# Performance work log

Hardware: AMD Instinct MI355X
Metric: run time of the kernel (lower is better)

## Reference

```python
import jax, jax.numpy as jnp
import numpy as np

B, T, HOP = 4, 200, 120
N = T * HOP
M1, A1 = 40, 5            # mcep_order+1, apdc_order+1
HID, COND = 256, 192
SR = 24000.0
ALPHA = 0.466             # frequency-warping for 24 kHz
PD = 4                    # Pade order
PADE = jnp.asarray([1.0, 0.4999273, 0.1067005, 0.00956526, 0.0003041358], jnp.float32)
SIGN = jnp.asarray([1.0, -1.0, 1.0, -1.0], jnp.float32)  # + for odd Pade tap index
F0_MEAN, F0_STD = 5.0, 0.25
MCEP_MEAN, MCEP_STD = 0.0, 1.0
APDC_MEAN, APDC_STD = 0.0, 1.0
NOISE_RATIO, SP_RATE, F0_RATE = 0.5, 1.0, 1.0


def mc2b(mc, a):
    """SPTK mc2b: mel-cepstrum -> MLSA filter coefficients (scan over order)."""
    mc_rev = jnp.moveaxis(mc, -1, 0)[::-1]  # [M1, B, T]
    def step(carry, c):
        b = c - a * carry
        return b, b
    _, bs = jax.lax.scan(step, jnp.zeros_like(mc_rev[0]), mc_rev)
    return jnp.moveaxis(bs[::-1], 0, -1)


def _mlsafir(x, b, d):
    # SPTK mlsafir, vectorized over the PD Pade taps.
    # x: [PD], b: [M1], d: [PD, M1+1]
    aa = 1.0 - ALPHA * ALPHA
    d1 = aa * x + ALPHA * d[:, 1]
    def step(prev, di):  # d_new[i] = d[i] + a*(d[i+1] - d_new[i-1]) : order recurrence
        d_i, d_ip1 = di
        new = d_i + ALPHA * (d_ip1 - prev)
        return new, new
    xs = (d[:, 2:M1].T, d[:, 3:M1 + 1].T)  # [M1-2, PD]
    _, dupd = jax.lax.scan(step, d1, xs)    # [M1-2, PD]
    y = jnp.einsum('mp,m->p', dupd, b[2:])
    # delay-line shift: new d = [x, d1, d1, dupd[2..M]]
    new_d = jnp.concatenate([x[:, None], d1[:, None], d1[:, None], dupd.T], axis=1)
    return y, new_d


def _mlsa_step(state, inp):
    d1a, d1b, d2, pt2 = state
    x, b = inp
    x = x * jnp.exp(b[0])           # gain
    # ---- stage 1 (uses b[1] only), SPTK mlsadf1 ----
    aa = 1.0 - ALPHA * ALPHA
    na = aa * d1b[:PD] + ALPHA * d1a[1:]
    npt = na * b[1]
    v1 = npt * PADE[1:]
    x1 = x + jnp.sum(v1 * SIGN)
    y1 = jnp.sum(v1) + x1
    d1a = jnp.concatenate([d1a[:1], na])
    d1b = jnp.concatenate([x1[None], npt])
    # ---- stage 2 (orders >= 2), SPTK mlsadf2 ----
    fy, d2 = _mlsafir(pt2[:PD], b, d2)
    v2 = fy * PADE[1:]
    x2 = y1 + jnp.sum(v2 * SIGN)
    y2 = jnp.sum(v2) + x2
    pt2 = jnp.concatenate([x2[None], fy])
    return (d1a, d1b, d2, pt2), y2


def mlsa_filter(exc, b_up):
    # exc: [N], b_up: [N, M1] -> filtered waveform [N]
    init = (jnp.zeros(PD + 1, jnp.float32), jnp.zeros(PD + 1, jnp.float32),
            jnp.zeros((PD, M1 + 1), jnp.float32), jnp.zeros(PD + 1, jnp.float32))
    _, y = jax.lax.scan(_mlsa_step, init, (exc, b_up))
    return y


def _forward(mceps, apdcs, frame_f0s, noise,
             Wm, bm, Wa, ba, Wf, bf, Wpa, bpa, Wpp, bpp,
             Wrp, brp, Wra, bra, Wap):
    # linear feature embed + sum
    hs = mceps @ Wm + bm + apdcs @ Wa + ba + frame_f0s @ Wf + bf   # [B,T,HID]
    ca = hs @ Wpa + bpa                                             # prenet_a cond [B,T,COND]
    cp = hs @ Wpp + bpp                                             # prenet_p cond
    # denorm (+ exp for log-f0)
    f0 = jnp.exp(frame_f0s[..., 0] * F0_STD + F0_MEAN) * F0_RATE    # [B,T]
    sp = mceps * MCEP_STD + MCEP_MEAN
    ap = apdcs * APDC_STD + APDC_MEAN
    # per-path mel-cepstra with prenet residuals
    mc_p = sp * SP_RATE + 0.1 * jnp.tanh(cp @ Wrp + brp)
    mc_a = sp * SP_RATE + 0.1 * jnp.tanh(ca @ Wra + bra) + ap @ Wap
    b_p = mc2b(mc_p, ALPHA)
    b_a = mc2b(mc_a, ALPHA)
    # excitation at sample rate
    f0_up = jnp.repeat(f0, HOP, axis=1)                             # [B,N]
    phase = jnp.cumsum(f0_up / SR, axis=1)
    w = jnp.floor(phase)
    wprev = jnp.concatenate([jnp.zeros_like(w[:, :1]), w[:, :-1]], axis=1)
    amp = jnp.sqrt(SR / jnp.maximum(f0_up, 1.0))
    pulse = jnp.where(w > wprev, amp, 0.0)
    exc_p = pulse * (1.0 - NOISE_RATIO)
    exc_a = noise * NOISE_RATIO
    # run both (periodic/aperiodic) MLSA synthesis filters in one batched scan
    excs = jnp.concatenate([exc_p, exc_a], axis=0)                  # [2B,N]
    bs = jnp.repeat(jnp.concatenate([b_p, b_a], axis=0), HOP, axis=1)  # [2B,N,M1]
    wavs = jax.vmap(mlsa_filter)(excs, bs)                          # [2B,N]
    return wavs[:B] + wavs[B:]


_forward_jit = jax.jit(_forward)


def setup_inputs() -> dict:
    key = jax.random.key(0)
    ks = jax.random.split(key, 20)
    decay = 0.3 / (1.0 + jnp.arange(M1, dtype=jnp.float32))  # realistic cepstral decay (filter stability)
    return {
        'mceps': jax.random.normal(ks[0], (B, T, M1), jnp.float32) * decay,
        'apdcs': jax.random.normal(ks[1], (B, T, A1), jnp.float32) * 0.3,
        'frame_f0s': jax.random.normal(ks[2], (B, T, 1), jnp.float32),
        'noise': jax.random.normal(ks[3], (B, N), jnp.float32),
        'Wm': jax.random.normal(ks[4], (M1, HID), jnp.float32) / np.sqrt(M1),
        'bm': jnp.zeros((HID,), jnp.float32),
        'Wa': jax.random.normal(ks[5], (A1, HID), jnp.float32) / np.sqrt(A1),
        'ba': jnp.zeros((HID,), jnp.float32),
        'Wf': jax.random.normal(ks[6], (1, HID), jnp.float32),
        'bf': jnp.zeros((HID,), jnp.float32),
        'Wpa': jax.random.normal(ks[7], (HID, COND), jnp.float32) / np.sqrt(HID),
        'bpa': jnp.zeros((COND,), jnp.float32),
        'Wpp': jax.random.normal(ks[8], (HID, COND), jnp.float32) / np.sqrt(HID),
        'bpp': jnp.zeros((COND,), jnp.float32),
        'Wrp': jax.random.normal(ks[9], (COND, M1), jnp.float32) / np.sqrt(COND),
        'brp': jnp.zeros((M1,), jnp.float32),
        'Wra': jax.random.normal(ks[10], (COND, M1), jnp.float32) / np.sqrt(COND),
        'bra': jnp.zeros((M1,), jnp.float32),
        'Wap': jax.random.normal(ks[11], (A1, M1), jnp.float32) * 0.05,
    }


def reference(mceps, apdcs, frame_f0s, noise,
              Wm, bm, Wa, ba, Wf, bf, Wpa, bpa, Wpp, bpp,
              Wrp, brp, Wra, bra, Wap):
    return _forward_jit(mceps, apdcs, frame_f0s, noise,
                        Wm, bm, Wa, ba, Wf, bf, Wpa, bpa, Wpp, bpp,
                        Wrp, brp, Wra, bra, Wap)
```

## Files before the change

kernel.cpp:

```cpp
#include <hip/hip_runtime.h>
#include <math.h>

#define ALPHA 0.466f
#define T_FRAMES 200
#define HOPW 120
#define NSAMP 24000
#define M1 40
#define HID 256
#define CONDW 192

#define WARMS 384
#define OUTS 96
#define SLOTS (NSAMP / OUTS)

#define F8 8
#define EMB_BLOCKS (4 * T_FRAMES / F8)
#define BPF ((NSAMP + 255) / 256)

#if defined(__has_builtin)
#  if __has_builtin(__builtin_amdgcn_permlane32_swap)
#    define HAVE_PLSWAP 1
#  endif
#endif
#ifndef HAVE_PLSWAP
#  define HAVE_PLSWAP 0
#endif

__global__ __launch_bounds__(256) void prep_kernel(
    const float* __restrict__ mceps, const float* __restrict__ apdcs,
    const float* __restrict__ f0s, const float* __restrict__ noise,
    const float* __restrict__ Wm, const float* __restrict__ bm,
    const float* __restrict__ Wa, const float* __restrict__ ba,
    const float* __restrict__ Wf, const float* __restrict__ bf,
    const float* __restrict__ Wpa, const float* __restrict__ bpa,
    const float* __restrict__ Wpp, const float* __restrict__ bpp,
    const float* __restrict__ Wrp, const float* __restrict__ brp,
    const float* __restrict__ Wra, const float* __restrict__ bra,
    const float* __restrict__ Wap,
    float* __restrict__ bcoef, float* __restrict__ exc)
{
    const int tid = threadIdx.x;

    if (blockIdx.x >= EMB_BLOCKS) {
        const int xb = blockIdx.x - EMB_BLOCKS;
        const int ff = xb / BPF;
        const int n = (xb % BPF) * 256 + tid;

        if (ff >= 4) {
            if (n < NSAMP) exc[ff * NSAMP + n] = 0.5f * noise[(ff - 4) * NSAMP + n];
            return;
        }

        __shared__ double s_base[T_FRAMES];
        __shared__ double s_step[T_FRAMES];
        __shared__ float  s_amp[T_FRAMES];

        if (tid < 64) {
            const int L = tid;
            double st[4], loc[4];
            float am[4];
            double s = 0.0;
            #pragma unroll
            for (int j = 0; j < 4; ++j) {
                int ft = L * 4 + j;
                if (ft < T_FRAMES) {
                    double fv = exp((double)f0s[ff * T_FRAMES + ft] * 0.25 + 5.0);
                    st[j] = fv / 24000.0;
                    am[j] = (float)(0.5 * sqrt(24000.0 / fmax(fv, 1.0)));
                } else { st[j] = 0.0; am[j] = 0.f; }
                loc[j] = s;
                s += st[j];
            }
            double tot = s;
            #pragma unroll
            for (int off = 1; off < 64; off <<= 1) {
                double v = __shfl_up(s, off, 64);
                if (L >= off) s += v;
            }
            double excl = s - tot;
            #pragma unroll
            for (int j = 0; j < 4; ++j) {
                int ft = L * 4 + j;
                if (ft < T_FRAMES) {
                    s_base[ft] = 120.0 * (excl + loc[j]);
                    s_step[ft] = st[j];
                    s_amp[ft]  = am[j];
                }
            }
        }
        __syncthreads();

        if (n < NSAMP) {
            int ft = n / HOPW, k = n - ft * HOPW;
            double st = s_step[ft], bs = s_base[ft];
            double ph  = bs + (double)(k + 1) * st;
            double php = bs + (double)k * st;
            exc[ff * NSAMP + n] = (floor(ph) > floor(php)) ? s_amp[ft] : 0.0f;
        }
        return;
    }

    __shared__ float s_mc[F8][M1];
    __shared__ float s_ap[F8][5];
    __shared__ float s_f0[F8];
    __shared__ float s_h[F8][HID];
    __shared__ float s_ca[F8][CONDW];
    __shared__ float s_cp[F8][CONDW];
    __shared__ float s_mcp[F8][M1];
    __shared__ float s_mca[F8][M1];

    const int R0 = blockIdx.x * F8;

    for (int j = tid; j < F8 * M1; j += 256) s_mc[j / M1][j % M1] = mceps[R0 * M1 + j];
    if (tid < F8 * 5) s_ap[tid / 5][tid % 5] = apdcs[R0 * 5 + tid];
    if (tid < F8)     s_f0[tid] = f0s[R0 + tid];
    __syncthreads();

    {
        float acc[F8];
        const float bias = bm[tid] + ba[tid] + bf[tid];
        #pragma unroll
        for (int r = 0; r < F8; ++r) acc[r] = bias;
        for (int k = 0; k < M1; ++k) {
            float w = Wm[k * HID + tid];
            #pragma unroll
            for (int r = 0; r < F8; ++r) acc[r] = fmaf(s_mc[r][k], w, acc[r]);
        }
        #pragma unroll
        for (int k = 0; k < 5; ++k) {
            float w = Wa[k * HID + tid];
            #pragma unroll
            for (int r = 0; r < F8; ++r) acc[r] = fmaf(s_ap[r][k], w, acc[r]);
        }
        float wf = Wf[tid];
        #pragma unroll
        for (int r = 0; r < F8; ++r) s_h[r][tid] = fmaf(s_f0[r], wf, acc[r]);
    }
    __syncthreads();

    if (tid < CONDW) {
        float aA[F8], aP[F8];
        #pragma unroll
        for (int r = 0; r < F8; ++r) { aA[r] = bpa[tid]; aP[r] = bpp[tid]; }
        for (int k = 0; k < HID; k += 4) {
            float4 h4[F8];
            #pragma unroll
            for (int r = 0; r < F8; ++r) h4[r] = *(const float4*)&s_h[r][k];
            #pragma unroll
            for (int kk = 0; kk < 4; ++kk) {
                float wa = Wpa[(k + kk) * CONDW + tid];
                float wp = Wpp[(k + kk) * CONDW + tid];
                #pragma unroll
                for (int r = 0; r < F8; ++r) {
                    float hv = (&h4[r].x)[kk];
                    aA[r] = fmaf(hv, wa, aA[r]);
                    aP[r] = fmaf(hv, wp, aP[r]);
                }
            }
        }
        #pragma unroll
        for (int r = 0; r < F8; ++r) { s_ca[r][tid] = aA[r]; s_cp[r][tid] = aP[r]; }
    }
    __syncthreads();

    if (tid < M1) {
        const int u = tid;
        float acc[F8];
        #pragma unroll
        for (int r = 0; r < F8; ++r) acc[r] = brp[u];
        for (int k = 0; k < CONDW; k += 4) {
            float4 c4[F8];
            #pragma unroll
            for (int r = 0; r < F8; ++r) c4[r] = *(const float4*)&s_cp[r][k];
            #pragma unroll
            for (int kk = 0; kk < 4; ++kk) {
                float w = Wrp[(k + kk) * M1 + u];
                #pragma unroll
                for (int r = 0; r < F8; ++r) acc[r] = fmaf((&c4[r].x)[kk], w, acc[r]);
            }
        }
        #pragma unroll
        for (int r = 0; r < F8; ++r)
            s_mcp[r][u] = s_mc[r][u] + 0.1f * tanhf(acc[r]);
    } else if (tid >= 64 && tid < 64 + M1) {
        const int u = tid - 64;
        float acc[F8];
        #pragma unroll
        for (int r = 0; r < F8; ++r) acc[r] = bra[u];
        for (int k = 0; k < CONDW; k += 4) {
            float4 c4[F8];
            #pragma unroll
            for (int r = 0; r < F8; ++r) c4[r] = *(const float4*)&s_ca[r][k];
            #pragma unroll
            for (int kk = 0; kk < 4; ++kk) {
                float w = Wra[(k + kk) * M1 + u];
                #pragma unroll
                for (int r = 0; r < F8; ++r) acc[r] = fmaf((&c4[r].x)[kk], w, acc[r]);
            }
        }
        #pragma unroll
        for (int r = 0; r < F8; ++r) {
            float aw = 0.f;
            #pragma unroll
            for (int j = 0; j < 5; ++j) aw = fmaf(s_ap[r][j], Wap[j * M1 + u], aw);
            s_mca[r][u] = s_mc[r][u] + 0.1f * tanhf(acc[r]) + aw;
        }
    }
    __syncthreads();

    if (tid < 16) {
        const int r = tid >> 1, path = tid & 1;
        const int R = R0 + r;
        const int batch = R / T_FRAMES, t = R - batch * T_FRAMES;
        const float* src = path ? s_mca[r] : s_mcp[r];
        float* dst = bcoef + ((path * 4 + batch) * T_FRAMES + t) * M1;
        float prev = src[M1 - 1];
        dst[M1 - 1] = prev;
        for (int m = M1 - 2; m >= 0; --m) {
            prev = src[m] - ALPHA * prev;
            dst[m] = prev;
        }
    }
}

template <int CTRL>
__device__ __forceinline__ float rshr(float x) {
    return __int_as_float(
        __builtin_amdgcn_mov_dpp(__float_as_int(x), CTRL, 0xF, 0xF, true));
}
__device__ __forceinline__ float rlane(float x, int l) {
    return __int_as_float(__builtin_amdgcn_readlane(__float_as_int(x), l));
}
__device__ __forceinline__ float vpin(float x) {
    asm("" : "+v"(x));
    return x;
}

__device__ __forceinline__ void run_frame(
    const float* __restrict__ sx, float AB,
    float BP1, float BP2, float BP3, float BP4,
    float B0, float B1, float B2, float B3, float B4,
    float K, float IPw, bool pos0, bool row0, bool parodd,
    float& E0, float& E1, float& E2, float& E3, float& E4,
    float& dlp, float& xin,
    float& m1, float& m2, float& m3, float& m4, float& w0,
    float* __restrict__ yb, int ks, int ke)
{
    const float A   = ALPHA;
    const float AA  = 1.0f - A * A;
    const float A2  = A * A;
    const float mA3 = -(A * A2);
    const float A4  = A2 * A2;
    const float R   = -(A4 * A);
    const float R2  = R * R;

    const float Rv   = vpin(R);
    const float R2v  = vpin(R2);
    const float IPwv = vpin(IPw);

    #pragma unroll 1
    for (int k8 = ks; k8 < ke; k8 += 8) {
        const float4 g0 = *(const float4*)&sx[k8];
        const float4 g1 = *(const float4*)&sx[k8 + 4];
        const float xs[8] = {g0.x, g0.y, g0.z, g0.w, g1.x, g1.y, g1.z, g1.w};
        #pragma unroll
        for (int j = 0; j < 8; ++j) {
            float x = xs[j];

            float na0 = fmaf(A, m1, AA * w0);
            float na1 = fmaf(A, m2, AB * m1);
            float na2 = fmaf(A, m3, AB * m2);
            float na3 = fmaf(A, m4, AB * m3);
            float p = fmaf(na2, BP3, na0 * BP1);
            float q = fmaf(na3, BP4, na1 * BP2);
            float x1 = x + (p - q);
            float y1 = fmaf(2.0f, p, x);
            m1 = na0; m2 = na1; m3 = na2; m4 = na3; w0 = x1;

            float pE4 = rshr<0x112>(E4);
            float c0 = fmaf(A, E0, pos0 ? dlp : pE4);
            float c1 = fmaf(A, E1, E0);
            float c2 = fmaf(A, E2, E1);
            float c3 = fmaf(A, E3, E2);
            float c4 = fmaf(A, E4, E3);
            float u0 = c0;
            float u1 = fmaf(-A, u0, c1);
            float u2 = fmaf(-A, u1, c2);
            float u3 = fmaf(-A, u2, c3);
            float u4 = fmaf(-A, u3, c4);
            float X = u4;
            X = fmaf(rshr<0x112>(X), Rv,  X);
            X = fmaf(rshr<0x114>(X), R2v, X);
            float dl = fmaf(AA, xin, A * dlp);
            float Xt = fmaf(K, dl, X);
            float Si = rshr<0x112>(Xt);
            Si = pos0 ? dl : Si;
            float t0 = fmaf(-A,  Si, u0);
            float t1 = fmaf(A2,  Si, u1);
            float t2 = fmaf(mA3, Si, u2);
            float t3 = fmaf(A4,  Si, u3);

            float fp = t0 * B0;
            fp = fmaf(t1, B1, fp);
            fp = fmaf(t2, B2, fp);
            fp = fmaf(t3, B3, fp);
            fp = fmaf(Xt, B4, fp);
            float S = fp;
            S += rshr<0x112>(S);
            S += rshr<0x114>(S);
            S += rshr<0x118>(S);

            float Sx  = rshr<0x111>(S);
            float T1m = rshr<0x142>(S)  * IPwv;
            float T0m = rshr<0x142>(Sx) * IPwv;
            float xprev = parodd ? T1m : T0m;

#if HAVE_PLSWAP
            typedef unsigned u32x2 __attribute__((ext_vector_type(2)));
            u32x2 rr = __builtin_amdgcn_permlane32_swap(
                __float_as_uint(S), __float_as_uint(S), false, false);
            float S2 = __uint_as_float(rr.x) + __uint_as_float(rr.y);
            float aE = rlane(S2, 14), bE = rlane(S2, 30);
            float aO = rlane(S2, 15), bO = rlane(S2, 31);
            float tot = parodd ? (aO + bO) : (aE + bE);
            float x2 = y1 + tot;
            float dif = parodd ? (aO - bO) : (aE - bE);
            yb[k8 + j] = x2 + dif;
#else
            float s0p = rlane(S, 14), s1p = rlane(S, 30);
            float s2p = rlane(S, 46), s3p = rlane(S, 62);
            float s0a = rlane(S, 15), s1a = rlane(S, 31);
            float s2a = rlane(S, 47), s3a = rlane(S, 63);
            float eP = s0p + s2p, oP = s1p + s3p;
            float eA = s0a + s2a, oA = s1a + s3a;
            float ce = parodd ? eA : eP;
            float co = parodd ? oA : oP;
            float x2 = y1 + (ce + co);
            yb[k8 + j] = x2 + (ce - co);
#endif

            xin = row0 ? x2 : xprev;
            E0 = t0; E1 = t1; E2 = t2; E3 = t3; E4 = Xt;
            dlp = dl;
        }
    }
}

__global__ __launch_bounds__(64) void mlsa_kernel(
    const float* __restrict__ bcoef, const float* __restrict__ exc,
    float* __restrict__ out)
{
    __shared__ __align__(16) float sexc[2][HOPW + 8];
    __shared__ __align__(16) float ybuf[2][HOPW + 8];

    const int tid = threadIdx.x;
    const int par = tid & 1;
    const int pos = (tid >> 1) & 7;
    const int row = tid >> 4;
    const int slot = blockIdx.x >> 2;
    const int b = blockIdx.x & 3;
    const int f = par * 4 + b;
    const bool pos0 = (pos == 0), row0 = (row == 0), parodd = (par != 0);

    const float P1 = 0.4999273f, P2 = 0.1067005f, P3 = 0.00956526f, P4 = 0.0003041358f;
    const float wrow = (row == 0) ? P1 : (row == 1) ? -P2 : (row == 2) ? P3 : -P4;
    const float IPw  = (row == 1) ? (1.f / P1) : (row == 2) ? (-1.f / P2)
                     : (row == 3) ? (1.f / P3) : 0.f;

    const float A = ALPHA;
    const float R = -(A * A * A * A * A);
    float K = R;
    for (int j = 0; j < pos; ++j) K *= R;

    float E0 = 0.f, E1 = 0.f, E2 = 0.f, E3 = 0.f, E4 = 0.f;
    float dlp = 0.f, xin = 0.f;
    float m1 = 0.f, m2 = 0.f, m3 = 0.f, m4 = 0.f, w0 = 0.f;

    const float* sxp = sexc[par];
    float* ybp = ybuf[par];
    const int ja = 5 * pos + 2;
    const int lh = tid >> 1;

    const int o0 = slot * OUTS;
    const int s0 = o0 - WARMS;
    const int fA = (s0 <= 0) ? 0 : (s0 / HOPW);
    const int fB = (o0 + OUTS - 1) / HOPW;

    #pragma unroll 1
    for (int ft = fA; ft <= fB; ++ft) {
        const float* bp = bcoef + (f * T_FRAMES + ft) * M1;
        const float b1 = bp[1];
        const float G  = expf(bp[0]);
        const float AAc = 1.0f - A * A;
        const float AB = AAc * b1;
        const float BP1 = b1 * P1, BP2 = b1 * P2, BP3 = b1 * P3, BP4 = b1 * P4;

        const float* ex = exc + f * NSAMP + ft * HOPW;
        #pragma unroll
        for (int m = 0; m < 4; ++m) {
            int kk = lh + 32 * m;
            if (kk < HOPW) sexc[par][kk] = ex[kk] * G;
        }

        const float B0c = bp[ja]     * wrow;
        const float B1c = bp[ja + 1] * wrow;
        const float B2c = bp[ja + 2] * wrow;
        const float B3c = (pos < 7) ? bp[ja + 3] * wrow : 0.f;
        const float B4c = (pos < 7) ? bp[ja + 4] * wrow : 0.f;

        int ks = s0 - ft * HOPW; if (ks < 0) ks = 0;
        int ke = o0 + OUTS - ft * HOPW; if (ke > HOPW) ke = HOPW;

        run_frame(sxp, AB, BP1, BP2, BP3, BP4,
                  B0c, B1c, B2c, B3c, B4c, K, IPw, pos0, row0, parodd,
                  E0, E1, E2, E3, E4, dlp, xin, m1, m2, m3, m4, w0,
                  ybp, ks, ke);

        int kout = o0 - ft * HOPW; if (kout < 0) kout = 0;
        if (kout < ke) {
            float* op = out + b * NSAMP + ft * HOPW;
            int i0 = kout + tid;
            if (i0 < ke) op[i0] = ybuf[0][i0] + ybuf[1][i0];
            int i1 = i0 + 64;
            if (i1 < ke) op[i1] = ybuf[0][i1] + ybuf[1][i1];
        }
    }
}

extern "C" void kernel_launch(void* const* d_in, const int* in_sizes, int n_in,
                              void* d_out, int out_size, void* d_ws, size_t ws_size,
                              hipStream_t stream) {
    const float* mceps = (const float*)d_in[0];
    const float* apdcs = (const float*)d_in[1];
    const float* f0s   = (const float*)d_in[2];
    const float* noise = (const float*)d_in[3];
    const float* Wm  = (const float*)d_in[4];
    const float* bm  = (const float*)d_in[5];
    const float* Wa  = (const float*)d_in[6];
    const float* ba  = (const float*)d_in[7];
    const float* Wf  = (const float*)d_in[8];
    const float* bf  = (const float*)d_in[9];
    const float* Wpa = (const float*)d_in[10];
    const float* bpa = (const float*)d_in[11];
    const float* Wpp = (const float*)d_in[12];
    const float* bpp = (const float*)d_in[13];
    const float* Wrp = (const float*)d_in[14];
    const float* brp = (const float*)d_in[15];
    const float* Wra = (const float*)d_in[16];
    const float* bra = (const float*)d_in[17];
    const float* Wap = (const float*)d_in[18];
    float* out = (float*)d_out;

    char* ws = (char*)d_ws;
    float* bcoef = (float*)(ws + 0);
    float* exc   = (float*)(ws + 256000);

    prep_kernel<<<dim3(EMB_BLOCKS + 8 * BPF), dim3(256), 0, stream>>>(
        mceps, apdcs, f0s, noise, Wm, bm, Wa, ba, Wf, bf,
        Wpa, bpa, Wpp, bpp, Wrp, brp, Wra, bra, Wap, bcoef, exc);

    mlsa_kernel<<<dim3(SLOTS * 4), dim3(64), 0, stream>>>(bcoef, exc, out);
}
```

Before: 195.6 us.

## Retime MLSA recurrence to precompute partial output sum off the critical path

Restructures the per-sample MLSA stage-2 recurrence so the bulk of the cross-lane output sum (SX) is computed from the previous sample's state. Only a single fma with the new input term remains on the serial dependency chain. Per-frame constants GB and CKp are folded into a precomputed correction, and the partial sum is recomputed at frame boundaries when coefficients change. The intent is a shorter latency chain per sample in this latency-bound scan, at the cost of extra setup per frame and more live registers. Shared buffer padding also shrinks.

```diff
diff --git a/kernel.cpp b/kernel.cpp
--- a/kernel.cpp
+++ b/kernel.cpp
@@ -240,8 +240,10 @@
     const float* __restrict__ sx, float AB,
     float BP1, float BP2, float BP3, float BP4,
     float B0, float B1, float B2, float B3, float B4,
-    float K, float IPw, bool pos0, bool row0, bool parodd,
-    float& E0, float& E1, float& E2, float& E3, float& E4,
+    float GB, float CKp, float K, float KS, float IPw,
+    bool pos0, bool row0, bool parodd,
+    float& uP0, float& uP1, float& uP2, float& uP3,
+    float& XP, float& XSP, float& SXP,
     float& dlp, float& xin,
     float& m1, float& m2, float& m3, float& m4, float& w0,
     float* __restrict__ yb, int ks, int ke)
@@ -267,6 +269,18 @@
         for (int j = 0; j < 8; ++j) {
             float x = xs[j];
 
+            float dl = fmaf(AA, xin, A * dlp);
+            float S  = fmaf(dl, CKp, SXP);
+
+            float Sx  = rshr<0x111>(S);
+            float TT1 = rshr<0x142>(S);
+            float TT0 = rshr<0x142>(Sx);
+#if HAVE_PLSWAP
+            typedef unsigned u32x2 __attribute__((ext_vector_type(2)));
+            u32x2 rr = __builtin_amdgcn_permlane32_swap(
+                __float_as_uint(S), __float_as_uint(S), false, false);
+#endif
+
             float na0 = fmaf(A, m1, AA * w0);
             float na1 = fmaf(A, m2, AB * m1);
             float na2 = fmaf(A, m3, AB * m2);
@@ -277,48 +291,40 @@
             float y1 = fmaf(2.0f, p, x);
             m1 = na0; m2 = na1; m3 = na2; m4 = na3; w0 = x1;
 
-            float pE4 = rshr<0x112>(E4);
-            float c0 = fmaf(A, E0, pos0 ? dlp : pE4);
-            float c1 = fmaf(A, E1, E0);
-            float c2 = fmaf(A, E2, E1);
-            float c3 = fmaf(A, E3, E2);
-            float c4 = fmaf(A, E4, E3);
+            float Si = fmaf(KS, dl, XSP);
+            float Xt = fmaf(K,  dl, XP);
+            float t0 = fmaf(-A,  Si, uP0);
+            float t1 = fmaf(A2,  Si, uP1);
+            float t2 = fmaf(mA3, Si, uP2);
+            float t3 = fmaf(A4,  Si, uP3);
+
+            float pE4 = rshr<0x112>(Xt);
+            float c0 = fmaf(A, t0, pos0 ? dl : pE4);
+            float c1 = fmaf(A, t1, t0);
+            float c2 = fmaf(A, t2, t1);
+            float c3 = fmaf(A, t3, t2);
+            float c4 = fmaf(A, Xt, t3);
             float u0 = c0;
             float u1 = fmaf(-A, u0, c1);
             float u2 = fmaf(-A, u1, c2);
             float u3 = fmaf(-A, u2, c3);
             float u4 = fmaf(-A, u3, c4);
-            float X = u4;
-            X = fmaf(rshr<0x112>(X), Rv,  X);
-            X = fmaf(rshr<0x114>(X), R2v, X);
-            float dl = fmaf(AA, xin, A * dlp);
-            float Xt = fmaf(K, dl, X);
-            float Si = rshr<0x112>(Xt);
-            Si = pos0 ? dl : Si;
-            float t0 = fmaf(-A,  Si, u0);
-            float t1 = fmaf(A2,  Si, u1);
-            float t2 = fmaf(mA3, Si, u2);
-            float t3 = fmaf(A4,  Si, u3);
-
-            float fp = t0 * B0;
-            fp = fmaf(t1, B1, fp);
-            fp = fmaf(t2, B2, fp);
-            fp = fmaf(t3, B3, fp);
-            fp = fmaf(Xt, B4, fp);
-            float S = fp;
-            S += rshr<0x112>(S);
-            S += rshr<0x114>(S);
-            S += rshr<0x118>(S);
-
-            float Sx  = rshr<0x111>(S);
-            float T1m = rshr<0x142>(S)  * IPwv;
-            float T0m = rshr<0x142>(Sx) * IPwv;
-            float xprev = parodd ? T1m : T0m;
+            float Xn = u4;
+            Xn = fmaf(rshr<0x112>(Xn), Rv,  Xn);
+            Xn = fmaf(rshr<0x114>(Xn), R2v, Xn);
+            float XSn = rshr<0x112>(Xn);
+            float fpX = u0 * B0;
+            fpX = fmaf(u1, B1, fpX);
+            fpX = fmaf(u2, B2, fpX);
+            fpX = fmaf(u3, B3, fpX);
+            fpX = fmaf(Xn, B4, fpX);
+            fpX = fmaf(XSn, GB, fpX);
+            float SXn = fpX;
+            SXn += rshr<0x112>(SXn);
+            SXn += rshr<0x114>(SXn);
+            SXn += rshr<0x118>(SXn);
 
 #if HAVE_PLSWAP
-            typedef unsigned u32x2 __attribute__((ext_vector_type(2)));
-            u32x2 rr = __builtin_amdgcn_permlane32_swap(
-                __float_as_uint(S), __float_as_uint(S), false, false);
             float S2 = __uint_as_float(rr.x) + __uint_as_float(rr.y);
             float aE = rlane(S2, 14), bE = rlane(S2, 30);
             float aO = rlane(S2, 15), bO = rlane(S2, 31);
@@ -338,9 +344,11 @@
             float x2 = y1 + (ce + co);
             yb[k8 + j] = x2 + (ce - co);
 #endif
-
+            float xprev = (parodd ? TT1 : TT0) * IPwv;
             xin = row0 ? x2 : xprev;
-            E0 = t0; E1 = t1; E2 = t2; E3 = t3; E4 = Xt;
+
+            uP0 = u0; uP1 = u1; uP2 = u2; uP3 = u3;
+            XP = Xn; XSP = XSn; SXP = SXn;
             dlp = dl;
         }
     }
@@ -350,8 +358,8 @@
     const float* __restrict__ bcoef, const float* __restrict__ exc,
     float* __restrict__ out)
 {
-    __shared__ __align__(16) float sexc[2][HOPW + 8];
-    __shared__ __align__(16) float ybuf[2][HOPW + 8];
+    __shared__ __align__(16) float sexc[2][HOPW + 4];
+    __shared__ __align__(16) float ybuf[2][HOPW + 4];
 
     const int tid = threadIdx.x;
     const int par = tid & 1;
@@ -368,11 +376,16 @@
                      : (row == 3) ? (1.f / P3) : 0.f;
 
     const float A = ALPHA;
-    const float R = -(A * A * A * A * A);
-    float K = R;
-    for (int j = 0; j < pos; ++j) K *= R;
-
-    float E0 = 0.f, E1 = 0.f, E2 = 0.f, E3 = 0.f, E4 = 0.f;
+    const float A2c = A * A;
+    const float mA3c = -(A * A2c);
+    const float A4c = A2c * A2c;
+    const float R = -(A4c * A);
+    float KS = 1.f;
+    for (int j = 0; j < pos; ++j) KS *= R;
+    const float K = KS * R;
+
+    float uP0 = 0.f, uP1 = 0.f, uP2 = 0.f, uP3 = 0.f;
+    float XP = 0.f, XSP = 0.f, SXP = 0.f;
     float dlp = 0.f, xin = 0.f;
     float m1 = 0.f, m2 = 0.f, m3 = 0.f, m4 = 0.f, w0 = 0.f;
 
@@ -408,12 +421,32 @@
         const float B3c = (pos < 7) ? bp[ja + 3] * wrow : 0.f;
         const float B4c = (pos < 7) ? bp[ja + 4] * wrow : 0.f;
 
+        const float GBc = fmaf(A4c, B3c, fmaf(mA3c, B2c, fmaf(A2c, B1c, -A * B0c)));
+        const float fpK = fmaf(K, B4c, KS * GBc);
+        float CKp = fpK;
+        CKp += rshr<0x112>(CKp);
+        CKp += rshr<0x114>(CKp);
+        CKp += rshr<0x118>(CKp);
+
+        float fpX0 = uP0 * B0c;
+        fpX0 = fmaf(uP1, B1c, fpX0);
+        fpX0 = fmaf(uP2, B2c, fpX0);
+        fpX0 = fmaf(uP3, B3c, fpX0);
+        fpX0 = fmaf(XP,  B4c, fpX0);
+        fpX0 = fmaf(XSP, GBc, fpX0);
+        SXP = fpX0;
+        SXP += rshr<0x112>(SXP);
+        SXP += rshr<0x114>(SXP);
+        SXP += rshr<0x118>(SXP);
+
         int ks = s0 - ft * HOPW; if (ks < 0) ks = 0;
         int ke = o0 + OUTS - ft * HOPW; if (ke > HOPW) ke = HOPW;
 
         run_frame(sxp, AB, BP1, BP2, BP3, BP4,
-                  B0c, B1c, B2c, B3c, B4c, K, IPw, pos0, row0, parodd,
-                  E0, E1, E2, E3, E4, dlp, xin, m1, m2, m3, m4, w0,
+                  B0c, B1c, B2c, B3c, B4c, GBc, CKp, K, KS, IPw,
+                  pos0, row0, parodd,
+                  uP0, uP1, uP2, uP3, XP, XSP, SXP,
+                  dlp, xin, m1, m2, m3, m4, w0,
                   ybp, ks, ke);
 
         int kout = o0 - ft * HOPW; if (kout < 0) kout = 0;
```

Result: slower. 199.9 us (+2.2%).

## Prefetch next frame's coefficients and excitation into double-buffered LDS, trim per-sample ops

Applied to the files above, without the earlier changes.

Loads the next frame's filter coefficients and excitation into registers before running the current frame. After the output store, it writes the gain-scaled excitation into a second LDS buffer, so global-load latency no longer sits on the serial per-frame path. The per-sample inner loop also changes in two ways. It drops the second cross-lane prefix step that used R^2, which is a numerical approximation that ignores a small higher-order term. It folds the final output into a single fma (y1 + 2a) instead of separate sum and difference terms. Keeping the prefetched values live adds register pressure, and dropping the R^2 term may perturb accuracy.

```diff
diff --git a/kernel.cpp b/kernel.cpp
--- a/kernel.cpp
+++ b/kernel.cpp
@@ -252,10 +252,8 @@
     const float mA3 = -(A * A2);
     const float A4  = A2 * A2;
     const float R   = -(A4 * A);
-    const float R2  = R * R;
 
     const float Rv   = vpin(R);
-    const float R2v  = vpin(R2);
     const float IPwv = vpin(IPw);
 
     #pragma unroll 1
@@ -289,8 +287,7 @@
             float u3 = fmaf(-A, u2, c3);
             float u4 = fmaf(-A, u3, c4);
             float X = u4;
-            X = fmaf(rshr<0x112>(X), Rv,  X);
-            X = fmaf(rshr<0x114>(X), R2v, X);
+            X = fmaf(rshr<0x112>(X), Rv, X);
             float dl = fmaf(AA, xin, A * dlp);
             float Xt = fmaf(K, dl, X);
             float Si = rshr<0x112>(Xt);
@@ -322,10 +319,10 @@
             float S2 = __uint_as_float(rr.x) + __uint_as_float(rr.y);
             float aE = rlane(S2, 14), bE = rlane(S2, 30);
             float aO = rlane(S2, 15), bO = rlane(S2, 31);
-            float tot = parodd ? (aO + bO) : (aE + bE);
-            float x2 = y1 + tot;
-            float dif = parodd ? (aO - bO) : (aE - bE);
-            yb[k8 + j] = x2 + dif;
+            float a  = parodd ? aO : aE;
+            float bb = parodd ? bO : bE;
+            float x2 = y1 + (a + bb);
+            yb[k8 + j] = fmaf(2.0f, a, y1);
 #else
             float s0p = rlane(S, 14), s1p = rlane(S, 30);
             float s2p = rlane(S, 46), s3p = rlane(S, 62);
@@ -336,7 +333,7 @@
             float ce = parodd ? eA : eP;
             float co = parodd ? oA : oP;
             float x2 = y1 + (ce + co);
-            yb[k8 + j] = x2 + (ce - co);
+            yb[k8 + j] = fmaf(2.0f, ce, y1);
 #endif
 
             xin = row0 ? x2 : xprev;
@@ -350,8 +347,8 @@
     const float* __restrict__ bcoef, const float* __restrict__ exc,
     float* __restrict__ out)
 {
-    __shared__ __align__(16) float sexc[2][HOPW + 8];
-    __shared__ __align__(16) float ybuf[2][HOPW + 8];
+    __shared__ __align__(16) float sexc[2][2][HOPW + 4];
+    __shared__ __align__(16) float ybuf[2][HOPW + 4];
 
     const int tid = threadIdx.x;
     const int par = tid & 1;
@@ -368,6 +365,7 @@
                      : (row == 3) ? (1.f / P3) : 0.f;
 
     const float A = ALPHA;
+    const float AAc = 1.0f - A * A;
     const float R = -(A * A * A * A * A);
     float K = R;
     for (int j = 0; j < pos; ++j) K *= R;
@@ -376,7 +374,6 @@
     float dlp = 0.f, xin = 0.f;
     float m1 = 0.f, m2 = 0.f, m3 = 0.f, m4 = 0.f, w0 = 0.f;
 
-    const float* sxp = sexc[par];
     float* ybp = ybuf[par];
     const int ja = 5 * pos + 2;
     const int lh = tid >> 1;
@@ -386,32 +383,48 @@
     const int fA = (s0 <= 0) ? 0 : (s0 / HOPW);
     const int fB = (o0 + OUTS - 1) / HOPW;
 
+    {
+        const float* bp0 = bcoef + (f * T_FRAMES + fA) * M1;
+        const float* ex0 = exc + f * NSAMP + fA * HOPW;
+        float G0 = expf(bp0[0]);
+        sexc[0][par][lh]      = ex0[lh]      * G0;
+        sexc[0][par][lh + 32] = ex0[lh + 32] * G0;
+        sexc[0][par][lh + 64] = ex0[lh + 64] * G0;
+        if (lh < HOPW - 96) sexc[0][par][lh + 96] = ex0[lh + 96] * G0;
+    }
+    const float* bpA = bcoef + (f * T_FRAMES + fA) * M1;
+    float b1c = bpA[1];
+    float AB  = AAc * b1c;
+    float BP1 = b1c * P1, BP2 = b1c * P2, BP3 = b1c * P3, BP4 = b1c * P4;
+    float B0c = bpA[ja]     * wrow;
+    float B1c = bpA[ja + 1] * wrow;
+    float B2c = bpA[ja + 2] * wrow;
+    float B3c = (pos < 7) ? bpA[ja + 3] * wrow : 0.f;
+    float B4c = (pos < 7) ? bpA[ja + 4] * wrow : 0.f;
+
+    int bufi = 0;
+
     #pragma unroll 1
     for (int ft = fA; ft <= fB; ++ft) {
-        const float* bp = bcoef + (f * T_FRAMES + ft) * M1;
-        const float b1 = bp[1];
-        const float G  = expf(bp[0]);
-        const float AAc = 1.0f - A * A;
-        const float AB = AAc * b1;
-        const float BP1 = b1 * P1, BP2 = b1 * P2, BP3 = b1 * P3, BP4 = b1 * P4;
-
-        const float* ex = exc + f * NSAMP + ft * HOPW;
-        #pragma unroll
-        for (int m = 0; m < 4; ++m) {
-            int kk = lh + 32 * m;
-            if (kk < HOPW) sexc[par][kk] = ex[kk] * G;
-        }
-
-        const float B0c = bp[ja]     * wrow;
-        const float B1c = bp[ja + 1] * wrow;
-        const float B2c = bp[ja + 2] * wrow;
-        const float B3c = (pos < 7) ? bp[ja + 3] * wrow : 0.f;
-        const float B4c = (pos < 7) ? bp[ja + 4] * wrow : 0.f;
+        const bool hasnext = (ft < fB);
+        const int ftn = hasnext ? ft + 1 : ft;
+
+        const float* bpn = bcoef + (f * T_FRAMES + ftn) * M1;
+        const float* exn = exc + f * NSAMP + ftn * HOPW;
+        float n_b0 = bpn[0];
+        float n_b1 = bpn[1];
+        float n_j0 = bpn[ja], n_j1 = bpn[ja + 1], n_j2 = bpn[ja + 2];
+        float n_j3 = (pos < 7) ? bpn[ja + 3] : 0.f;
+        float n_j4 = (pos < 7) ? bpn[ja + 4] : 0.f;
+        float ne0 = exn[lh];
+        float ne1 = exn[lh + 32];
+        float ne2 = exn[lh + 64];
+        float ne3 = (lh < HOPW - 96) ? exn[lh + 96] : 0.f;
 
         int ks = s0 - ft * HOPW; if (ks < 0) ks = 0;
         int ke = o0 + OUTS - ft * HOPW; if (ke > HOPW) ke = HOPW;
 
-        run_frame(sxp, AB, BP1, BP2, BP3, BP4,
+        run_frame(sexc[bufi][par], AB, BP1, BP2, BP3, BP4,
                   B0c, B1c, B2c, B3c, B4c, K, IPw, pos0, row0, parodd,
                   E0, E1, E2, E3, E4, dlp, xin, m1, m2, m3, m4, w0,
                   ybp, ks, ke);
@@ -423,6 +436,23 @@
             if (i0 < ke) op[i0] = ybuf[0][i0] + ybuf[1][i0];
             int i1 = i0 + 64;
             if (i1 < ke) op[i1] = ybuf[0][i1] + ybuf[1][i1];
+        }
+
+        if (hasnext) {
+            const int nb = bufi ^ 1;
+            float Gn = expf(n_b0);
+            sexc[nb][par][lh]      = ne0 * Gn;
+            sexc[nb][par][lh + 32] = ne1 * Gn;
+            sexc[nb][par][lh + 64] = ne2 * Gn;
+            if (lh < HOPW - 96) sexc[nb][par][lh + 96] = ne3 * Gn;
+            AB  = AAc * n_b1;
+            BP1 = n_b1 * P1; BP2 = n_b1 * P2; BP3 = n_b1 * P3; BP4 = n_b1 * P4;
+            B0c = n_j0 * wrow;
+            B1c = n_j1 * wrow;
+            B2c = n_j2 * wrow;
+            B3c = n_j3 * wrow;
+            B4c = n_j4 * wrow;
+            bufi = nb;
         }
     }
 }
```

After: 190.2 us. 1.03x faster.
